# Kernel tuning notes

Measured on AMD Instinct MI355X. Metric: run time of the kernel, lower is better.

The kernel has to match this reference:

```python
import jax, jax.numpy as jnp
import numpy as np

BEV = 128          # bev_res
EMBED = 128        # embed_dim
HEADS = 8
POINTS = 4
HD = EMBED // HEADS  # head dim = 16


def setup_inputs() -> dict:
    key = jax.random.key(0)
    ks = jax.random.split(key, 9)
    bs, nq = 4, BEV * BEV
    s = lambda k, shape: jax.random.normal(k, shape, jnp.float32) * 0.02
    return {
        "query": jax.random.normal(ks[0], (bs, nq, EMBED), jnp.float32),
        "W_off": s(ks[1], (EMBED, HEADS * POINTS * 2)),
        "b_off": s(ks[2], (HEADS * POINTS * 2,)),
        "W_attn": s(ks[3], (EMBED, HEADS * POINTS)),
        "b_attn": s(ks[4], (HEADS * POINTS,)),
        "W_val": s(ks[5], (EMBED, EMBED)),
        "b_val": s(ks[6], (EMBED,)),
        "W_out": s(ks[7], (EMBED, EMBED)),
        "b_out": s(ks[8], (EMBED,)),
    }


def _ref_points():
    # matches np.meshgrid(linspace(0,1,BEV), linspace(0,1,BEV), indexing='ij');
    # stacked as (col, row) = (x, y), flattened row-major to (BEV*BEV, 2)
    lin = jnp.linspace(0.0, 1.0, BEV)
    gy, gx = jnp.meshgrid(lin, lin, indexing="ij")
    return jnp.stack([gx, gy], axis=-1).reshape(-1, 2)


def _msda(query, W_off, b_off, W_attn, b_attn, W_val, b_val, W_out, b_out):
    bs, nq, _ = query.shape
    H = W = BEV
    # value projection; single level so num_value == nq == H*W
    value = query @ W_val + b_val
    v = value.reshape(bs, nq, HEADS, HD).transpose(0, 2, 1, 3)  # (bs, heads, HW, hd)

    # sampling offsets and attention weights (softmax over levels*points = points)
    off = (query @ W_off + b_off).reshape(bs, nq, HEADS, POINTS, 2)
    aw = jax.nn.softmax((query @ W_attn + b_attn).reshape(bs, nq, HEADS, POINTS), axis=-1)

    ref = _ref_points()  # (nq, 2) in [0,1], (x, y)
    norm = jnp.array([W, H], jnp.float32)  # offset_normalizer = (W, H)
    loc = ref[None, :, None, None, :] + off / norm  # (bs, nq, heads, pts, 2)

    # grid_sample bilinear, align_corners=False, padding_mode='zeros'
    px = loc[..., 0] * W - 0.5
    py = loc[..., 1] * H - 0.5
    x0 = jnp.floor(px)
    y0 = jnp.floor(py)
    wx = px - x0  # weight toward x0+1
    wy = py - y0
    x0i = x0.astype(jnp.int32)
    y0i = y0.astype(jnp.int32)

    def flat(a):  # (bs, nq, heads, pts) -> (bs, heads, nq*pts)
        return a.transpose(0, 2, 1, 3).reshape(bs, HEADS, nq * POINTS)

    def samp(xi, yi):
        valid = ((xi >= 0) & (xi < W) & (yi >= 0) & (yi < H)).astype(v.dtype)
        xc = jnp.clip(xi, 0, W - 1)
        yc = jnp.clip(yi, 0, H - 1)
        idx = flat(yc * W + xc)  # (bs, heads, nq*pts)
        g = jnp.take_along_axis(v, idx[..., None], axis=2)  # (bs, heads, nq*pts, hd)
        return g * flat(valid)[..., None]

    s00 = samp(x0i, y0i)
    s01 = samp(x0i + 1, y0i)
    s10 = samp(x0i, y0i + 1)
    s11 = samp(x0i + 1, y0i + 1)
    wxf = flat(wx)[..., None]
    wyf = flat(wy)[..., None]
    sampled = (s00 * (1 - wxf) * (1 - wyf) + s01 * wxf * (1 - wyf)
               + s10 * (1 - wxf) * wyf + s11 * wxf * wyf)
    sampled = sampled.reshape(bs, HEADS, nq, POINTS, HD)

    awt = aw.transpose(0, 2, 1, 3)  # (bs, heads, nq, pts)
    out = jnp.einsum("bhnpd,bhnp->bnhd", sampled, awt).reshape(bs, nq, EMBED)
    out = out @ W_out + b_out
    # mmcv MSDA adds identity (=query) internally; SelfAttention adds residual again
    return out + 2.0 * query


def reference(query, W_off, b_off, W_attn, b_attn, W_val, b_val, W_out, b_out):
    return _msda(query, W_off, b_off, W_attn, b_attn, W_val, b_val, W_out, b_out)
```

## Files before the change

### kernel.cpp

```cpp
#include <hip/hip_runtime.h>

#define BS 4
#define NQ 16384

typedef unsigned short u16;
typedef unsigned int u32;
typedef unsigned char u8;
typedef __attribute__((ext_vector_type(8))) short bf16x8;
typedef __attribute__((ext_vector_type(4))) short bf16x4;
typedef __attribute__((ext_vector_type(4))) float f32x4;
typedef __attribute__((ext_vector_type(2))) float f32x2;

__device__ __forceinline__ float bf2f(u16 v) { return __uint_as_float(((u32)v) << 16); }
__device__ __forceinline__ u16 f2bf(float f) {
    u32 u = __float_as_uint(f);
    return (u16)((u + 0x7fffu + ((u >> 16) & 1u)) >> 16);
}
__device__ __forceinline__ u32 pk_trunc(float lo, float hi) {
    return __builtin_amdgcn_perm(__float_as_uint(hi), __float_as_uint(lo), 0x07060302u);
}

union ABu { bf16x8 v; u32 u[4]; };

__global__ __launch_bounds__(256)
void setup_kernel(const float* __restrict__ W_val, const float* __restrict__ W_off,
                  const float* __restrict__ W_attn, const float* __restrict__ W_out,
                  u16* __restrict__ Wswz, u16* __restrict__ Wout_swz)
{
    const int i = blockIdx.x * 256 + threadIdx.x;
    if (i < 28672) {
        const int j = i & 7, lane = (i >> 3) & 15, quad = (i >> 7) & 3;
        const int kb = (i >> 9) & 3, nt = i >> 11;
        const int k = kb * 32 + quad * 8 + j;
        const int n = nt * 16 + lane;
        float v;
        if (n < 128)      v = W_val[k * 128 + n];
        else if (n < 192) v = W_off[k * 64 + (n - 128)];
        else              v = W_attn[k * 32 + (n - 192)];
        Wswz[i] = f2bf(v);
    } else if (i < 45056) {
        const int i2 = i - 28672;
        const int j = i2 & 7, lane = (i2 >> 3) & 15, quad = (i2 >> 7) & 3;
        const int kb = (i2 >> 9) & 3, nt = i2 >> 11;
        const int k = kb * 32 + quad * 8 + j;
        const int n = nt * 16 + lane;
        Wout_swz[i2] = f2bf(W_out[k * 128 + n]);
    }
}

__global__ __launch_bounds__(256, 4)
void fused_kernel(const float* __restrict__ query,
                  const float* __restrict__ b_off, const float* __restrict__ b_attn,
                  const float* __restrict__ b_val, const float* __restrict__ b_out,
                  const u16* __restrict__ Wswz, const u16* __restrict__ Wout_swz,
                  float* __restrict__ out)
{
    __shared__ __align__(16) u8  vhalo[144 * 144];
    __shared__ __align__(16) u16 scratch[64 * 136];

    const int tid = threadIdx.x;
    const int bid = blockIdx.x;
    const int xcd = bid & 7;
    const int ii  = bid >> 3;
    const int b_  = xcd >> 1;
    const int Y   = (((xcd & 1) << 3) | (ii >> 4)) << 3;
    const int X   = (ii & 15) << 3;

    const int w = tid >> 6, l = tid & 63;
    const int lane16 = l & 15, quad = l >> 4;
    const size_t batch_base = (size_t)b_ * NQ;

    const bf16x8* Wf  = (const bf16x8*)Wswz;
    const bf16x8* WfO = (const bf16x8*)Wout_swz;

    {
        const int tl = w * 16 + lane16;
        const float* qrow = query +
            (batch_base + (size_t)(Y + (tl >> 3)) * 128 + (X + (tl & 7))) * 128 + quad * 8;
        bf16x8 qfrag[4];
        #pragma unroll
        for (int kb = 0; kb < 4; ++kb) {
            f32x4 q0 = *(const f32x4*)(qrow + kb * 32);
            f32x4 q1 = *(const f32x4*)(qrow + kb * 32 + 4);
            ABu ab;
            ab.u[0] = pk_trunc(q0.x, q0.y); ab.u[1] = pk_trunc(q0.z, q0.w);
            ab.u[2] = pk_trunc(q1.x, q1.y); ab.u[3] = pk_trunc(q1.z, q1.w);
            qfrag[kb] = ab.v;
        }
        #pragma unroll
        for (int ntile = 0; ntile < 6; ++ntile) {
            const int nt = 8 + ntile;
            f32x4 acc = {0.f, 0.f, 0.f, 0.f};
            const bf16x8* wp = Wf + ((size_t)(nt * 4) * 4 + quad) * 16 + lane16;
            #pragma unroll
            for (int kb = 0; kb < 4; ++kb)
                acc = __builtin_amdgcn_mfma_f32_16x16x32_bf16(wp[kb * 64], qfrag[kb], acc, 0, 0, 0);
            const int c = ntile * 16 + quad * 4;
            const float4 bias = (ntile < 4) ? *(const float4*)&b_off[c]
                                            : *(const float4*)&b_attn[c - 64];
            uint2 pk;
            pk.x = pk_trunc(acc[0] + bias.x, acc[1] + bias.y);
            pk.y = pk_trunc(acc[2] + bias.z, acc[3] + bias.w);
            *(uint2*)&scratch[tl * 96 + c] = pk;
        }
    }

    #pragma unroll
    for (int i = 0; i < 3; ++i) {
        const int a = w + 4 * i;
        if (a >= 9) break;
        const int hp = a * 16 + lane16;
        const int hy = hp / 12, hx = hp - hy * 12;
        const int gy = min(max(Y - 2 + hy, 0), 127);
        const int gx = min(max(X - 2 + hx, 0), 127);
        const float* qrow = query + (batch_base + (size_t)gy * 128 + gx) * 128 + quad * 8;
        bf16x8 qfrag[4];
        #pragma unroll
        for (int kb = 0; kb < 4; ++kb) {
            f32x4 q0 = *(const f32x4*)(qrow + kb * 32);
            f32x4 q1 = *(const f32x4*)(qrow + kb * 32 + 4);
            ABu ab;
            ab.u[0] = pk_trunc(q0.x, q0.y); ab.u[1] = pk_trunc(q0.z, q0.w);
            ab.u[2] = pk_trunc(q1.x, q1.y); ab.u[3] = pk_trunc(q1.z, q1.w);
            qfrag[kb] = ab.v;
        }
        #pragma unroll
        for (int mt = 0; mt < 8; ++mt) {
            f32x4 acc = {0.f, 0.f, 0.f, 0.f};
            const bf16x8* wp = Wf + ((size_t)(mt * 4) * 4 + quad) * 16 + lane16;
            #pragma unroll
            for (int kb = 0; kb < 4; ++kb)
                acc = __builtin_amdgcn_mfma_f32_16x16x32_bf16(wp[kb * 64], qfrag[kb], acc, 0, 0, 0);
            const int d0 = mt * 16 + quad * 4;
            const float4 bias = *(const float4*)&b_val[d0];
            u32 pk = __builtin_amdgcn_cvt_pk_fp8_f32(acc[0] + bias.x, acc[1] + bias.y, 0, false);
            pk     = __builtin_amdgcn_cvt_pk_fp8_f32(acc[2] + bias.z, acc[3] + bias.w, pk, true);
            *(u32*)&vhalo[hp * 144 + d0] = pk;
        }
    }
    __syncthreads();

    float aw[2][4], ox[2][4], oy[2][4];
    #pragma unroll
    for (int it = 0; it < 2; ++it) {
        const int item = it * 256 + tid;
        const int t = item >> 3, h = item & 7;
        bf16x8 ofr = *(const bf16x8*)&scratch[t * 96 + h * 8];
        bf16x4 atr = *(const bf16x4*)&scratch[t * 96 + 64 + h * 4];
        #pragma unroll
        for (int p = 0; p < 4; ++p) {
            ox[it][p] = bf2f((u16)ofr[2 * p]);
            oy[it][p] = bf2f((u16)ofr[2 * p + 1]);
        }
        const float l0 = bf2f((u16)atr[0]), l1 = bf2f((u16)atr[1]);
        const float l2 = bf2f((u16)atr[2]), l3 = bf2f((u16)atr[3]);
        const float m = fmaxf(fmaxf(l0, l1), fmaxf(l2, l3));
        const float e0 = __expf(l0 - m), e1 = __expf(l1 - m);
        const float e2 = __expf(l2 - m), e3 = __expf(l3 - m);
        const float inv = 1.0f / (e0 + e1 + e2 + e3);
        aw[it][0] = e0 * inv; aw[it][1] = e1 * inv;
        aw[it][2] = e2 * inv; aw[it][3] = e3 * inv;
    }
    __syncthreads();

    #pragma unroll
    for (int it = 0; it < 2; ++it) {
        const int item = it * 256 + tid;
        const int t = item >> 3, h = item & 7;
        const int qx = X + (t & 7), qy = Y + (t >> 3);
        const float cx = (float)qx * (128.0f / 127.0f);
        const float cy = (float)qy * (128.0f / 127.0f);

        f32x2 acc2[8];
        #pragma unroll
        for (int d = 0; d < 8; ++d) acc2[d] = (f32x2){0.f, 0.f};

        #pragma unroll
        for (int p = 0; p < 4; ++p) {
            const float px = cx + ox[it][p] - 0.5f;
            const float py = cy + oy[it][p] - 0.5f;
            const float fx = floorf(px), fy = floorf(py);
            const float wx = px - fx, wy = py - fy;
            const int xi = (int)fx, yi = (int)fy;
            const float cw[4] = {(1.f - wx) * (1.f - wy), wx * (1.f - wy),
                                 (1.f - wx) * wy,         wx * wy};
            const int hx0 = min(max(xi - X + 2, 0), 11), hx1 = min(hx0 + 1, 11);
            const int hy0 = min(max(yi - Y + 2, 0), 11), hy1 = min(hy0 + 1, 11);
            const int cxs[4] = {hx0, hx1, hx0, hx1};
            const int cys[4] = {hy0, hy0, hy1, hy1};
            const int gxs[4] = {xi, xi + 1, xi, xi + 1};
            const int gys[4] = {yi, yi, yi + 1, yi + 1};
            #pragma unroll
            for (int c4 = 0; c4 < 4; ++c4) {
                const bool valid = (gxs[c4] >= 0) & (gxs[c4] < 128) &
                                   (gys[c4] >= 0) & (gys[c4] < 128);
                const float wgt = valid ? cw[c4] * aw[it][p] : 0.f;
                const f32x2 w2 = {wgt, wgt};
                const int hp = cys[c4] * 12 + cxs[c4];
                const int4 rv = *(const int4*)&vhalo[hp * 144 + h * 16];
                acc2[0] += w2 * __builtin_amdgcn_cvt_pk_f32_fp8(rv.x, false);
                acc2[1] += w2 * __builtin_amdgcn_cvt_pk_f32_fp8(rv.x, true);
                acc2[2] += w2 * __builtin_amdgcn_cvt_pk_f32_fp8(rv.y, false);
                acc2[3] += w2 * __builtin_amdgcn_cvt_pk_f32_fp8(rv.y, true);
                acc2[4] += w2 * __builtin_amdgcn_cvt_pk_f32_fp8(rv.z, false);
                acc2[5] += w2 * __builtin_amdgcn_cvt_pk_f32_fp8(rv.z, true);
                acc2[6] += w2 * __builtin_amdgcn_cvt_pk_f32_fp8(rv.w, false);
                acc2[7] += w2 * __builtin_amdgcn_cvt_pk_f32_fp8(rv.w, true);
            }
        }
        uint4 s0, s1;
        s0.x = pk_trunc(acc2[0][0], acc2[0][1]); s0.y = pk_trunc(acc2[1][0], acc2[1][1]);
        s0.z = pk_trunc(acc2[2][0], acc2[2][1]); s0.w = pk_trunc(acc2[3][0], acc2[3][1]);
        s1.x = pk_trunc(acc2[4][0], acc2[4][1]); s1.y = pk_trunc(acc2[5][0], acc2[5][1]);
        s1.z = pk_trunc(acc2[6][0], acc2[6][1]); s1.w = pk_trunc(acc2[7][0], acc2[7][1]);
        *(uint4*)&scratch[t * 136 + h * 16]     = s0;
        *(uint4*)&scratch[t * 136 + h * 16 + 8] = s1;
    }
    __syncthreads();

    {
        bf16x8 afrag[4];
        #pragma unroll
        for (int kb = 0; kb < 4; ++kb)
            afrag[kb] = *(const bf16x8*)&scratch[(w * 16 + lane16) * 136 + kb * 32 + quad * 8];

        #pragma unroll
        for (int nt = 0; nt < 8; ++nt) {
            f32x4 acc = {0.f, 0.f, 0.f, 0.f};
            const bf16x8* bp = WfO + ((size_t)(nt * 4) * 4 + quad) * 16 + lane16;
            #pragma unroll
            for (int kb = 0; kb < 4; ++kb)
                acc = __builtin_amdgcn_mfma_f32_16x16x32_bf16(afrag[kb], bp[kb * 64], acc, 0, 0, 0);
            const int n = nt * 16 + lane16;
            const float bias = b_out[n];
            #pragma unroll
            for (int r = 0; r < 4; ++r) {
                const int tl = w * 16 + quad * 4 + r;
                const size_t grow = batch_base + (size_t)(Y + (tl >> 3)) * 128 + (X + (tl & 7));
                const float q = query[grow * 128 + n];
                out[grow * 128 + n] = acc[r] + bias + 2.0f * q;
            }
        }
    }
}

extern "C" void kernel_launch(void* const* d_in, const int* in_sizes, int n_in,
                              void* d_out, int out_size, void* d_ws, size_t ws_size,
                              hipStream_t stream)
{
    const float* query  = (const float*)d_in[0];
    const float* W_off  = (const float*)d_in[1];
    const float* b_off  = (const float*)d_in[2];
    const float* W_attn = (const float*)d_in[3];
    const float* b_attn = (const float*)d_in[4];
    const float* W_val  = (const float*)d_in[5];
    const float* b_val  = (const float*)d_in[6];
    const float* W_out  = (const float*)d_in[7];
    const float* b_out  = (const float*)d_in[8];
    float* out = (float*)d_out;

    u16* Wswz     = (u16*)d_ws;
    u16* Wout_swz = (u16*)((char*)d_ws + 28672 * 2);

    setup_kernel<<<176, 256, 0, stream>>>(W_val, W_off, W_attn, W_out, Wswz, Wout_swz);
    fused_kernel<<<1024, 256, 0, stream>>>(query, b_off, b_attn, b_val, b_out,
                                           Wswz, Wout_swz, out);
}
```

Before: 137.5 us.

## Shrink query tile to 8x4 with smaller halo and more resident blocks

Halves each block's tile from 8x8 to 8x4 queries, doubling the grid to 2048 blocks. The value halo becomes 12x8, which cuts LDS use per block, and the launch-bounds occupancy hint rises from 4 to 7. Work is redistributed so four waves split the projection GEMM N-tiles and the halo value rows between them. The intent is higher occupancy and better latency hiding. The cost is more redundant halo value-projection compute relative to useful work, since the halo-to-tile ratio grows.

```diff
diff --git a/kernel.cpp b/kernel.cpp
--- a/kernel.cpp
+++ b/kernel.cpp
@@ -48,22 +48,22 @@
     }
 }
 
-__global__ __launch_bounds__(256, 4)
+__global__ __launch_bounds__(256, 7)
 void fused_kernel(const float* __restrict__ query,
                   const float* __restrict__ b_off, const float* __restrict__ b_attn,
                   const float* __restrict__ b_val, const float* __restrict__ b_out,
                   const u16* __restrict__ Wswz, const u16* __restrict__ Wout_swz,
                   float* __restrict__ out)
 {
-    __shared__ __align__(16) u8  vhalo[144 * 144];
-    __shared__ __align__(16) u16 scratch[64 * 136];
+    __shared__ __align__(16) u8  vhalo[96 * 144];
+    __shared__ __align__(16) u16 scratch[32 * 136];
 
     const int tid = threadIdx.x;
     const int bid = blockIdx.x;
     const int xcd = bid & 7;
     const int ii  = bid >> 3;
     const int b_  = xcd >> 1;
-    const int Y   = (((xcd & 1) << 3) | (ii >> 4)) << 3;
+    const int Y   = ((((xcd & 1) << 4) | (ii >> 4)) << 2);
     const int X   = (ii & 15) << 3;
 
     const int w = tid >> 6, l = tid & 63;
@@ -74,7 +74,8 @@
     const bf16x8* WfO = (const bf16x8*)Wout_swz;
 
     {
-        const int tl = w * 16 + lane16;
+        const int m = w & 1;
+        const int tl = m * 16 + lane16;
         const float* qrow = query +
             (batch_base + (size_t)(Y + (tl >> 3)) * 128 + (X + (tl & 7))) * 128 + quad * 8;
         bf16x8 qfrag[4];
@@ -87,17 +88,19 @@
             ab.u[2] = pk_trunc(q1.x, q1.y); ab.u[3] = pk_trunc(q1.z, q1.w);
             qfrag[kb] = ab.v;
         }
-        #pragma unroll
-        for (int ntile = 0; ntile < 6; ++ntile) {
-            const int nt = 8 + ntile;
+        const int unit0 = (w >> 1) * 3;
+        #pragma unroll
+        for (int nn = 0; nn < 3; ++nn) {
+            const int unit = unit0 + nn;
+            const int nt = 8 + unit;
             f32x4 acc = {0.f, 0.f, 0.f, 0.f};
             const bf16x8* wp = Wf + ((size_t)(nt * 4) * 4 + quad) * 16 + lane16;
             #pragma unroll
             for (int kb = 0; kb < 4; ++kb)
                 acc = __builtin_amdgcn_mfma_f32_16x16x32_bf16(wp[kb * 64], qfrag[kb], acc, 0, 0, 0);
-            const int c = ntile * 16 + quad * 4;
-            const float4 bias = (ntile < 4) ? *(const float4*)&b_off[c]
-                                            : *(const float4*)&b_attn[c - 64];
+            const int c = unit * 16 + quad * 4;
+            const float4 bias = (unit < 4) ? *(const float4*)&b_off[c]
+                                           : *(const float4*)&b_attn[c - 64];
             uint2 pk;
             pk.x = pk_trunc(acc[0] + bias.x, acc[1] + bias.y);
             pk.y = pk_trunc(acc[2] + bias.z, acc[3] + bias.w);
@@ -105,52 +108,55 @@
         }
     }
 
-    #pragma unroll
-    for (int i = 0; i < 3; ++i) {
-        const int a = w + 4 * i;
-        if (a >= 9) break;
-        const int hp = a * 16 + lane16;
-        const int hy = hp / 12, hx = hp - hy * 12;
-        const int gy = min(max(Y - 2 + hy, 0), 127);
-        const int gx = min(max(X - 2 + hx, 0), 127);
-        const float* qrow = query + (batch_base + (size_t)gy * 128 + gx) * 128 + quad * 8;
-        bf16x8 qfrag[4];
-        #pragma unroll
-        for (int kb = 0; kb < 4; ++kb) {
-            f32x4 q0 = *(const f32x4*)(qrow + kb * 32);
-            f32x4 q1 = *(const f32x4*)(qrow + kb * 32 + 4);
-            ABu ab;
-            ab.u[0] = pk_trunc(q0.x, q0.y); ab.u[1] = pk_trunc(q0.z, q0.w);
-            ab.u[2] = pk_trunc(q1.x, q1.y); ab.u[3] = pk_trunc(q1.z, q1.w);
-            qfrag[kb] = ab.v;
-        }
-        #pragma unroll
-        for (int mt = 0; mt < 8; ++mt) {
-            f32x4 acc = {0.f, 0.f, 0.f, 0.f};
-            const bf16x8* wp = Wf + ((size_t)(mt * 4) * 4 + quad) * 16 + lane16;
-            #pragma unroll
-            for (int kb = 0; kb < 4; ++kb)
-                acc = __builtin_amdgcn_mfma_f32_16x16x32_bf16(wp[kb * 64], qfrag[kb], acc, 0, 0, 0);
-            const int d0 = mt * 16 + quad * 4;
-            const float4 bias = *(const float4*)&b_val[d0];
-            u32 pk = __builtin_amdgcn_cvt_pk_fp8_f32(acc[0] + bias.x, acc[1] + bias.y, 0, false);
-            pk     = __builtin_amdgcn_cvt_pk_fp8_f32(acc[2] + bias.z, acc[3] + bias.w, pk, true);
-            *(u32*)&vhalo[hp * 144 + d0] = pk;
+    {
+        const int pt_a = w + (w >> 1);
+        #pragma unroll
+        for (int seg = 0; seg < 2; ++seg) {
+            const int pt   = pt_a + seg;
+            const int mtlo = seg ? 0 : ((w & 1) * 4);
+            const int mthi = seg ? ((w & 1) ? 8 : 4) : 8;
+            const int hp = pt * 16 + lane16;
+            const int hy = hp / 12, hx = hp - hy * 12;
+            const int gy = min(max(Y - 2 + hy, 0), 127);
+            const int gx = min(max(X - 2 + hx, 0), 127);
+            const float* qrow = query + (batch_base + (size_t)gy * 128 + gx) * 128 + quad * 8;
+            bf16x8 qfrag[4];
+            #pragma unroll
+            for (int kb = 0; kb < 4; ++kb) {
+                f32x4 q0 = *(const f32x4*)(qrow + kb * 32);
+                f32x4 q1 = *(const f32x4*)(qrow + kb * 32 + 4);
+                ABu ab;
+                ab.u[0] = pk_trunc(q0.x, q0.y); ab.u[1] = pk_trunc(q0.z, q0.w);
+                ab.u[2] = pk_trunc(q1.x, q1.y); ab.u[3] = pk_trunc(q1.z, q1.w);
+                qfrag[kb] = ab.v;
+            }
+            #pragma unroll
+            for (int mt = 0; mt < 8; ++mt) {
+                if (mt < mtlo || mt >= mthi) continue;
+                f32x4 acc = {0.f, 0.f, 0.f, 0.f};
+                const bf16x8* wp = Wf + ((size_t)(mt * 4) * 4 + quad) * 16 + lane16;
+                #pragma unroll
+                for (int kb = 0; kb < 4; ++kb)
+                    acc = __builtin_amdgcn_mfma_f32_16x16x32_bf16(wp[kb * 64], qfrag[kb], acc, 0, 0, 0);
+                const int d0 = mt * 16 + quad * 4;
+                const float4 bias = *(const float4*)&b_val[d0];
+                u32 pk = __builtin_amdgcn_cvt_pk_fp8_f32(acc[0] + bias.x, acc[1] + bias.y, 0, false);
+                pk     = __builtin_amdgcn_cvt_pk_fp8_f32(acc[2] + bias.z, acc[3] + bias.w, pk, true);
+                *(u32*)&vhalo[hp * 144 + d0] = pk;
+            }
         }
     }
     __syncthreads();
 
-    float aw[2][4], ox[2][4], oy[2][4];
-    #pragma unroll
-    for (int it = 0; it < 2; ++it) {
-        const int item = it * 256 + tid;
-        const int t = item >> 3, h = item & 7;
-        bf16x8 ofr = *(const bf16x8*)&scratch[t * 96 + h * 8];
-        bf16x4 atr = *(const bf16x4*)&scratch[t * 96 + 64 + h * 4];
+    const int t_it = tid >> 3, h_it = tid & 7;
+    float aw[4], ox[4], oy[4];
+    {
+        bf16x8 ofr = *(const bf16x8*)&scratch[t_it * 96 + h_it * 8];
+        bf16x4 atr = *(const bf16x4*)&scratch[t_it * 96 + 64 + h_it * 4];
         #pragma unroll
         for (int p = 0; p < 4; ++p) {
-            ox[it][p] = bf2f((u16)ofr[2 * p]);
-            oy[it][p] = bf2f((u16)ofr[2 * p + 1]);
+            ox[p] = bf2f((u16)ofr[2 * p]);
+            oy[p] = bf2f((u16)ofr[2 * p + 1]);
         }
         const float l0 = bf2f((u16)atr[0]), l1 = bf2f((u16)atr[1]);
         const float l2 = bf2f((u16)atr[2]), l3 = bf2f((u16)atr[3]);
@@ -158,16 +164,12 @@
         const float e0 = __expf(l0 - m), e1 = __expf(l1 - m);
         const float e2 = __expf(l2 - m), e3 = __expf(l3 - m);
         const float inv = 1.0f / (e0 + e1 + e2 + e3);
-        aw[it][0] = e0 * inv; aw[it][1] = e1 * inv;
-        aw[it][2] = e2 * inv; aw[it][3] = e3 * inv;
+        aw[0] = e0 * inv; aw[1] = e1 * inv; aw[2] = e2 * inv; aw[3] = e3 * inv;
     }
     __syncthreads();
 
-    #pragma unroll
-    for (int it = 0; it < 2; ++it) {
-        const int item = it * 256 + tid;
-        const int t = item >> 3, h = item & 7;
-        const int qx = X + (t & 7), qy = Y + (t >> 3);
+    {
+        const int qx = X + (t_it & 7), qy = Y + (t_it >> 3);
         const float cx = (float)qx * (128.0f / 127.0f);
         const float cy = (float)qy * (128.0f / 127.0f);
 
@@ -177,15 +179,15 @@
 
         #pragma unroll
         for (int p = 0; p < 4; ++p) {
-            const float px = cx + ox[it][p] - 0.5f;
-            const float py = cy + oy[it][p] - 0.5f;
+            const float px = cx + ox[p] - 0.5f;
+            const float py = cy + oy[p] - 0.5f;
             const float fx = floorf(px), fy = floorf(py);
             const float wx = px - fx, wy = py - fy;
             const int xi = (int)fx, yi = (int)fy;
             const float cw[4] = {(1.f - wx) * (1.f - wy), wx * (1.f - wy),
                                  (1.f - wx) * wy,         wx * wy};
             const int hx0 = min(max(xi - X + 2, 0), 11), hx1 = min(hx0 + 1, 11);
-            const int hy0 = min(max(yi - Y + 2, 0), 11), hy1 = min(hy0 + 1, 11);
+            const int hy0 = min(max(yi - Y + 2, 0), 7),  hy1 = min(hy0 + 1, 7);
             const int cxs[4] = {hx0, hx1, hx0, hx1};
             const int cys[4] = {hy0, hy0, hy1, hy1};
             const int gxs[4] = {xi, xi + 1, xi, xi + 1};
@@ -194,10 +196,10 @@
             for (int c4 = 0; c4 < 4; ++c4) {
                 const bool valid = (gxs[c4] >= 0) & (gxs[c4] < 128) &
                                    (gys[c4] >= 0) & (gys[c4] < 128);
-                const float wgt = valid ? cw[c4] * aw[it][p] : 0.f;
+                const float wgt = valid ? cw[c4] * aw[p] : 0.f;
                 const f32x2 w2 = {wgt, wgt};
                 const int hp = cys[c4] * 12 + cxs[c4];
-                const int4 rv = *(const int4*)&vhalo[hp * 144 + h * 16];
+                const int4 rv = *(const int4*)&vhalo[hp * 144 + h_it * 16];
                 acc2[0] += w2 * __builtin_amdgcn_cvt_pk_f32_fp8(rv.x, false);
                 acc2[1] += w2 * __builtin_amdgcn_cvt_pk_f32_fp8(rv.x, true);
                 acc2[2] += w2 * __builtin_amdgcn_cvt_pk_f32_fp8(rv.y, false);
@@ -213,19 +215,22 @@
         s0.z = pk_trunc(acc2[2][0], acc2[2][1]); s0.w = pk_trunc(acc2[3][0], acc2[3][1]);
         s1.x = pk_trunc(acc2[4][0], acc2[4][1]); s1.y = pk_trunc(acc2[5][0], acc2[5][1]);
         s1.z = pk_trunc(acc2[6][0], acc2[6][1]); s1.w = pk_trunc(acc2[7][0], acc2[7][1]);
-        *(uint4*)&scratch[t * 136 + h * 16]     = s0;
-        *(uint4*)&scratch[t * 136 + h * 16 + 8] = s1;
+        *(uint4*)&scratch[t_it * 136 + h_it * 16]     = s0;
+        *(uint4*)&scratch[t_it * 136 + h_it * 16 + 8] = s1;
     }
     __syncthreads();
 
     {
+        const int m = w & 1;
         bf16x8 afrag[4];
         #pragma unroll
         for (int kb = 0; kb < 4; ++kb)
-            afrag[kb] = *(const bf16x8*)&scratch[(w * 16 + lane16) * 136 + kb * 32 + quad * 8];
-
-        #pragma unroll
-        for (int nt = 0; nt < 8; ++nt) {
+            afrag[kb] = *(const bf16x8*)&scratch[(m * 16 + lane16) * 136 + kb * 32 + quad * 8];
+
+        const int nt0 = (w >> 1) * 4;
+        #pragma unroll
+        for (int nn = 0; nn < 4; ++nn) {
+            const int nt = nt0 + nn;
             f32x4 acc = {0.f, 0.f, 0.f, 0.f};
             const bf16x8* bp = WfO + ((size_t)(nt * 4) * 4 + quad) * 16 + lane16;
             #pragma unroll
@@ -235,7 +240,7 @@
             const float bias = b_out[n];
             #pragma unroll
             for (int r = 0; r < 4; ++r) {
-                const int tl = w * 16 + quad * 4 + r;
+                const int tl = m * 16 + quad * 4 + r;
                 const size_t grow = batch_base + (size_t)(Y + (tl >> 3)) * 128 + (X + (tl & 7));
                 const float q = query[grow * 128 + n];
                 out[grow * 128 + n] = acc[r] + bias + 2.0f * q;
@@ -263,6 +268,6 @@
     u16* Wout_swz = (u16*)((char*)d_ws + 28672 * 2);
 
     setup_kernel<<<176, 256, 0, stream>>>(W_val, W_off, W_attn, W_out, Wswz, Wout_swz);
-    fused_kernel<<<1024, 256, 0, stream>>>(query, b_off, b_attn, b_val, b_out,
+    fused_kernel<<<2048, 256, 0, stream>>>(query, b_off, b_attn, b_val, b_out,
                                            Wswz, Wout_swz, out);
 }
```

After: 149.9 us. +9.0%, slower.
